# Optimization experiments

Hardware: AMD Instinct MI355X
Metric: run time of the kernel (lower is better)

## Reference

```python
import jax, jax.numpy as jnp
import numpy as np

THRESH = 1e-5   # replace_denormals threshold
EPS = 1e-5      # instance_norm eps

NUM_LAYERS, TOKEN_LEN, EMBED = 24, 100, 1024
N, B = 1025, 8  # seq (incl. cls token), batch


def _replace_denormals(x):
    return jnp.where((x < THRESH) & (x > -THRESH), THRESH, x)


def _delta_feat(feats, tokens, w_t2f, b_t2f, w_df, b_df, instance_norm):
    # feats: [n, b, c], tokens: [m, c]
    attn = jnp.einsum('nbc,mc->nbm', feats, tokens)
    if instance_norm:  # normalize over m per (n, b), biased variance (torch F.instance_norm)
        mu = attn.mean(axis=-1, keepdims=True)
        var = attn.var(axis=-1, keepdims=True)
        attn = (attn - mu) / jnp.sqrt(var + EPS)
    attn = jax.nn.softmax(attn * (feats.shape[-1] ** -0.5), axis=-1)
    v = tokens[1:] @ w_t2f.T + b_t2f                     # [m-1, c]
    df = jnp.einsum('nbm,mc->nbc', attn[:, :, 1:], v)    # drop first token column
    return (df + feats) @ w_df.T + b_df


def setup_inputs() -> dict:
    key = jax.random.key(0)
    ks = jax.random.split(key, 12)
    C = EMBED
    inp = {
        'feats': jax.random.normal(ks[0], (N, B, C), dtype=jnp.float32),
        'learnable_tokens': jax.random.normal(ks[1], (NUM_LAYERS, TOKEN_LEN, C), dtype=jnp.float32) * 0.04,
        'learnable_tokens2': jax.random.normal(ks[2], (NUM_LAYERS, TOKEN_LEN, C), dtype=jnp.float32) * 0.04,
        'w_t2f': jax.random.normal(ks[3], (C, C), dtype=jnp.float32) * 0.02,
        'b_t2f': jax.random.normal(ks[4], (C,), dtype=jnp.float32) * 0.02,
        'w_df': jax.random.normal(ks[5], (C, C), dtype=jnp.float32) * 0.02,
        'b_df': jax.random.normal(ks[6], (C,), dtype=jnp.float32) * 0.02,
        'w_t2f2': jax.random.normal(ks[7], (C, C), dtype=jnp.float32) * 0.02,
        'b_t2f2': jax.random.normal(ks[8], (C,), dtype=jnp.float32) * 0.02,
        'w_df2': jax.random.normal(ks[9], (C, C), dtype=jnp.float32) * 0.02,
        'b_df2': jax.random.normal(ks[10], (C,), dtype=jnp.float32) * 0.02,
        'scale': jnp.float32(0.001),
        'layer': 0,
    }
    return inp


def reference(feats, learnable_tokens, learnable_tokens2,
              w_t2f, b_t2f, w_df, b_df,
              w_t2f2, b_t2f2, w_df2, b_df2,
              scale, layer):
    # batch_first=False, has_cls_token=True (defaults)
    C = feats.shape[-1]
    cls_tok, x = feats[:1], feats[1:]            # [1,b,c], [n,b,c]
    n, b = x.shape[0], x.shape[1]

    # decompose: fft2 over last two dims (b, c), norm='backward'
    f = jnp.fft.fft2(x)
    re, im = jnp.real(f), jnp.imag(f)
    amp = jnp.sqrt(_replace_denormals(re * re + im * im))
    phase = jnp.arctan2(im, _replace_denormals(re))

    t1 = learnable_tokens[layer]
    t2 = learnable_tokens2[layer]
    d_phase = _delta_feat(phase, t1, w_t2f, b_t2f, w_df, b_df, instance_norm=False)
    d_amp = _delta_feat(amp, t2, w_t2f2, b_t2f2, w_df2, b_df2, instance_norm=True)

    # compose: stacked last dim has size 2, dim 2 has size C -> divide by sqrt(C*2)
    z = (jnp.cos(d_phase) * d_amp + 1j * (jnp.sin(d_phase) * d_amp)) / np.float32(np.sqrt(C * 2.0))
    z = z[..., : C // 2 + 1]                      # torch irfft2 trims last dim to s[-1]//2+1
    delta = jnp.fft.irfft2(z, s=(b, C), norm='ortho')

    out = x + delta * scale
    return jnp.concatenate([cls_tok, out], axis=0)
```

## Files before the change

### kernel.cpp

```cpp
#include <hip/hip_runtime.h>
#include <cstddef>


using bf16x8 = __attribute__((ext_vector_type(8))) short;
using f32x4  = __attribute__((ext_vector_type(4))) float;

__device__ inline short f2bf(float f) {
  union { float f; unsigned u; } v; v.f = f;
  unsigned r = v.u + 0x7FFFu + ((v.u >> 16) & 1u);
  return (short)(r >> 16);
}
__device__ inline float bf2f(short s) {
  union { unsigned u; float f; } v; v.u = ((unsigned)(unsigned short)s) << 16;
  return v.f;
}
__device__ inline void async16(const void* g, void* l) {
  __builtin_amdgcn_global_load_lds(
      (const __attribute__((address_space(1))) void*)g,
      (__attribute__((address_space(3))) void*)l, 16, 0, 0);
}
__device__ inline float fast_atan2(float y, float x) {
  float ax = fabsf(x), ay = fabsf(y);
  float mx = fmaxf(ax, ay), mn = fminf(ax, ay);
  float a = mn * __frcp_rn(mx);
  float s = a * a;
  float r = fmaf(fmaf(fmaf(-0.0464964749f, s, 0.15931422f), s, -0.327622764f),
                 s * a, a);
  if (ay > ax) r = 1.5707963267948966f - r;
  if (x < 0.f) r = 3.14159265358979f - r;
  return (y < 0.f) ? -r : r;
}

__device__ inline int PADi(int i) { return i + (i >> 5); }
__device__ inline int rev4_8(int t) {
  return ((t & 3) << 6) | (((t >> 2) & 3) << 4) | (((t >> 4) & 3) << 2) | ((t >> 6) & 3);
}

template <int SIGN>
__device__ inline void fft1024x4(float2 (*zb)[1056], int t) {
#pragma unroll
  for (int s = 0; s < 5; ++s) {
    const int Q = 256 >> (2 * s);
    const int j = t & (Q - 1);
    const int i0 = ((t & ~(Q - 1)) << 2) + j;
    const float ang = (float)SIGN * 6.283185307179586f * (float)j / (float)(4 * Q);
    float s1, c1; __sincosf(ang, &s1, &c1);
    const float c2 = c1 * c1 - s1 * s1, s2 = 2.f * c1 * s1;
    const float c3 = c2 * c1 - s2 * s1, s3 = c2 * s1 + s2 * c1;
#pragma unroll
    for (int p = 0; p < 4; ++p) {
      float2* z = zb[p];
      float2 x0 = z[PADi(i0)];
      float2 x1 = z[PADi(i0 + Q)];
      float2 x2 = z[PADi(i0 + 2 * Q)];
      float2 x3 = z[PADi(i0 + 3 * Q)];
      float t0x = x0.x + x2.x, t0y = x0.y + x2.y;
      float t1x = x0.x - x2.x, t1y = x0.y - x2.y;
      float t2x = x1.x + x3.x, t2y = x1.y + x3.y;
      float t3x = x1.x - x3.x, t3y = x1.y - x3.y;
      float u0x = t0x + t2x, u0y = t0y + t2y;
      float u2x = t0x - t2x, u2y = t0y - t2y;
      float u1x, u1y, u3x, u3y;
      if (SIGN < 0) { u1x = t1x + t3y; u1y = t1y - t3x; u3x = t1x - t3y; u3y = t1y + t3x; }
      else          { u1x = t1x - t3y; u1y = t1y + t3x; u3x = t1x + t3y; u3y = t1y - t3x; }
      z[PADi(i0)]         = make_float2(u0x, u0y);
      z[PADi(i0 + Q)]     = make_float2(u1x * c1 - u1y * s1, u1x * s1 + u1y * c1);
      z[PADi(i0 + 2 * Q)] = make_float2(u2x * c2 - u2y * s2, u2x * s2 + u2y * c2);
      z[PADi(i0 + 3 * Q)] = make_float2(u3x * c3 - u3y * s3, u3x * s3 + u3y * c3);
    }
    __syncthreads();
  }
}

__global__ __launch_bounds__(256) void fwd_fft2_amp(const float* __restrict__ feats,
                                                    short* __restrict__ ampb,
                                                    short* __restrict__ phaseb) {
  __shared__ float2 zb[4][1056];
  const int t = threadIdx.x;
  const int n = blockIdx.x;
  const float* base = feats + 8192 + (size_t)n * 8192;
#pragma unroll
  for (int p = 0; p < 4; ++p) {
    const float* x0 = base + (size_t)(2 * p) * 1024;
    const float* x1 = x0 + 1024;
#pragma unroll
    for (int m = 0; m < 4; ++m) {
      const int c = t + 256 * m;
      zb[p][PADi(c)] = make_float2(x0[c], x1[c]);
    }
  }
  __syncthreads();
  fft1024x4<-1>(zb, t);
  const int rt = rev4_8(t);
  const float cv[8] = {1.f, 0.70710678f, 0.f, -0.70710678f, -1.f, -0.70710678f, 0.f, 0.70710678f};
  const float sv[8] = {0.f, 0.70710678f, 1.f, 0.70710678f, 0.f, -0.70710678f, -1.f, -0.70710678f};
  short* ab = ampb + (size_t)n * 8192;
  short* pb = phaseb + (size_t)n * 8192;
#pragma unroll
  for (int m = 0; m < 4; ++m) {
    const int k = 256 * m + t;
    const int kk = (1024 - k) & 1023;
    const int pos  = 4 * rt + m;
    const int pos2 = 4 * rev4_8(kk & 255) + (kk >> 8);
    float xr[8], xi[8];
#pragma unroll
    for (int p = 0; p < 4; ++p) {
      float2 Z = zb[p][PADi(pos)];
      float2 W = zb[p][PADi(pos2)];
      xr[2 * p]     = 0.5f * (Z.x + W.x);
      xi[2 * p]     = 0.5f * (Z.y - W.y);
      xr[2 * p + 1] = 0.5f * (Z.y + W.y);
      xi[2 * p + 1] = 0.5f * (W.x - Z.x);
    }
#pragma unroll
    for (int kb = 0; kb < 8; ++kb) {
      float sr = 0.f, si = 0.f;
#pragma unroll
      for (int b = 0; b < 8; ++b) {
        const int p = (kb * b) & 7;
        sr += xr[b] * cv[p] + xi[b] * sv[p];
        si += xi[b] * cv[p] - xr[b] * sv[p];
      }
      float r2 = sr * sr + si * si;
      if (r2 < 1e-5f) r2 = 1e-5f;
      float a = sqrtf(r2);
      float rr = (sr < 1e-5f && sr > -1e-5f) ? 1e-5f : sr;
      float ph = fast_atan2(si, rr);
      ab[kb * 1024 + k] = f2bf(a);
      pb[kb * 1024 + k] = f2bf(ph);
    }
  }
}

__global__ __launch_bounds__(256) void conv_all(
    const float* __restrict__ w1, const float* __restrict__ w2,
    const float* __restrict__ w3, const float* __restrict__ w4,
    const float* __restrict__ lt1, const float* __restrict__ lt2,
    const int* __restrict__ layerp, const float* __restrict__ feats,
    short* __restrict__ Wdst, short* __restrict__ Tdst,
    float* __restrict__ out) {
  const int id = blockIdx.x;
  const int t = threadIdx.x * 4;
  if (id < 4096) {
    const int z = id >> 10, row = id & 1023;
    const float* W = (z == 0 ? w1 : z == 1 ? w2 : z == 2 ? w3 : w4)
                     + (size_t)row * 1024;
    short* D = Wdst + ((size_t)z * 1024 + row) * 1024;
    float4 v = *(const float4*)(W + t);
    D[t] = f2bf(v.x); D[t + 1] = f2bf(v.y); D[t + 2] = f2bf(v.z); D[t + 3] = f2bf(v.w);
  } else if (id < 4608) {
    const int i2 = id - 4096;
    const int zz = i2 >> 7, row = i2 & 127;
    const int z = zz & 1, shift = zz >> 1;
    short* D = Tdst + ((size_t)zz * 128 + row) * 1024;
    if (row + shift < 100) {
      const float* S = (z ? lt2 : lt1) + (size_t)layerp[0] * 102400
                       + (size_t)(row + shift) * 1024;
      float4 v = *(const float4*)(S + t);
      D[t] = f2bf(v.x); D[t + 1] = f2bf(v.y); D[t + 2] = f2bf(v.z); D[t + 3] = f2bf(v.w);
    } else {
      D[t] = 0; D[t + 1] = 0; D[t + 2] = 0; D[t + 3] = 0;
    }
  } else {
    const int i = (id - 4608) * 256 + threadIdx.x;
    out[i] = feats[i];
  }
}

__global__ __launch_bounds__(256) void gemm128(
    const short* A0, const short* A1,
    const short* B0, const short* B1,
    const short* Add0, const short* Add1,
    const float* bias0, const float* bias1,
    void* C0v, void* C1v,
    int K, int ldc, int outBf16, int biasMode) {
  const int z = blockIdx.z;
  const short* A   = z ? A1 : A0;
  const short* B   = z ? B1 : B0;
  const short* Add = z ? Add1 : Add0;
  const float* bias = z ? bias1 : bias0;
  void* Cv = z ? C1v : C0v;

  __shared__ __align__(16) short As[128 * 32];
  __shared__ __align__(16) short Bs[128 * 32];

  const int tid = threadIdx.x;
  const int wave = tid >> 6, lane = tid & 63;
  const int m16 = lane & 15, quad = lane >> 4;
  const int wm = (wave & 1) * 64, wn = (wave >> 1) * 64;

  f32x4 acc[4][4];
#pragma unroll
  for (int i = 0; i < 4; ++i)
#pragma unroll
    for (int j = 0; j < 4; ++j) acc[i][j] = (f32x4){0.f, 0.f, 0.f, 0.f};

  const int r0 = tid >> 2;
  const int csw = (((tid & 3) ^ ((r0 >> 1) & 3)) * 8);
  const short* aSrc0 = A + (size_t)(blockIdx.x * 128 + r0) * K + csw;
  const short* aSrc1 = aSrc0 + (size_t)64 * K;
  const short* bSrc0 = B + (size_t)(blockIdx.y * 128 + r0) * K + csw;
  const short* bSrc1 = bSrc0 + (size_t)64 * K;
  short* aDst0 = As + tid * 8;
  short* aDst1 = As + 2048 + tid * 8;
  short* bDst0 = Bs + tid * 8;
  short* bDst1 = Bs + 2048 + tid * 8;

  const int fcol = ((quad ^ ((m16 >> 1) & 3)) * 8) + m16 * 32;

  for (int k0 = 0; k0 < K; k0 += 32) {
    async16(aSrc0 + k0, aDst0);
    async16(aSrc1 + k0, aDst1);
    async16(bSrc0 + k0, bDst0);
    async16(bSrc1 + k0, bDst1);
    __syncthreads();
    bf16x8 af[4], bg[4];
#pragma unroll
    for (int ib = 0; ib < 4; ++ib)
      af[ib] = *(const bf16x8*)(As + (wm + ib * 16) * 32 + fcol);
#pragma unroll
    for (int jb = 0; jb < 4; ++jb)
      bg[jb] = *(const bf16x8*)(Bs + (wn + jb * 16) * 32 + fcol);
#pragma unroll
    for (int ib = 0; ib < 4; ++ib)
#pragma unroll
      for (int jb = 0; jb < 4; ++jb)
        acc[ib][jb] = __builtin_amdgcn_mfma_f32_16x16x32_bf16(af[ib], bg[jb], acc[ib][jb], 0, 0, 0);
    __syncthreads();
  }

#pragma unroll
  for (int ib = 0; ib < 4; ++ib) {
    const int rowb = blockIdx.x * 128 + wm + ib * 16 + quad * 4;
#pragma unroll
    for (int jb = 0; jb < 4; ++jb) {
      const int col = blockIdx.y * 128 + wn + jb * 16 + m16;
      const float bcv = (biasMode == 1) ? bias[col] : 0.f;
#pragma unroll
      for (int r = 0; r < 4; ++r) {
        const size_t idx = (size_t)(rowb + r) * (size_t)ldc + col;
        float v = acc[ib][jb][r] + bcv;
        if (biasMode == 2) v += bias[rowb + r];
        if (Add) v += bf2f(Add[idx]);
        if (outBf16) ((short*)Cv)[idx] = f2bf(v);
        else         ((float*)Cv)[idx] = v;
      }
    }
  }
}

__global__ __launch_bounds__(256) void gemm128_dual(
    const short* A1_0, const short* A1_1,
    const short* B1_0, const short* B1_1,
    const short* A2_0, const short* A2_1,
    const short* B2_0, const short* B2_1,
    const float* bias0, const float* bias1,
    short* C0, short* C1, int K1, int K2, int ldc) {
  const int z = blockIdx.z;
  const short* A1 = z ? A1_1 : A1_0;
  const short* B1 = z ? B1_1 : B1_0;
  const short* A2 = z ? A2_1 : A2_0;
  const short* B2 = z ? B2_1 : B2_0;
  const float* bias = z ? bias1 : bias0;
  short* C = z ? C1 : C0;

  __shared__ __align__(16) short As[128 * 32];
  __shared__ __align__(16) short Bs[128 * 32];

  const int tid = threadIdx.x;
  const int wave = tid >> 6, lane = tid & 63;
  const int m16 = lane & 15, quad = lane >> 4;
  const int wm = (wave & 1) * 64, wn = (wave >> 1) * 64;

  f32x4 acc[4][4];
#pragma unroll
  for (int i = 0; i < 4; ++i)
#pragma unroll
    for (int j = 0; j < 4; ++j) acc[i][j] = (f32x4){0.f, 0.f, 0.f, 0.f};

  const int r0 = tid >> 2;
  const int csw = (((tid & 3) ^ ((r0 >> 1) & 3)) * 8);
  short* aDst0 = As + tid * 8;
  short* aDst1 = As + 2048 + tid * 8;
  short* bDst0 = Bs + tid * 8;
  short* bDst1 = Bs + 2048 + tid * 8;
  const int fcol = ((quad ^ ((m16 >> 1) & 3)) * 8) + m16 * 32;

#pragma unroll 1
  for (int phase = 0; phase < 2; ++phase) {
    const short* A = phase ? A2 : A1;
    const short* B = phase ? B2 : B1;
    const int K = phase ? K2 : K1;
    const short* aSrc0 = A + (size_t)(blockIdx.x * 128 + r0) * K + csw;
    const short* aSrc1 = aSrc0 + (size_t)64 * K;
    const short* bSrc0 = B + (size_t)(blockIdx.y * 128 + r0) * K + csw;
    const short* bSrc1 = bSrc0 + (size_t)64 * K;
    for (int k0 = 0; k0 < K; k0 += 32) {
      async16(aSrc0 + k0, aDst0);
      async16(aSrc1 + k0, aDst1);
      async16(bSrc0 + k0, bDst0);
      async16(bSrc1 + k0, bDst1);
      __syncthreads();
      bf16x8 af[4], bg[4];
#pragma unroll
      for (int ib = 0; ib < 4; ++ib)
        af[ib] = *(const bf16x8*)(As + (wm + ib * 16) * 32 + fcol);
#pragma unroll
      for (int jb = 0; jb < 4; ++jb)
        bg[jb] = *(const bf16x8*)(Bs + (wn + jb * 16) * 32 + fcol);
#pragma unroll
      for (int ib = 0; ib < 4; ++ib)
#pragma unroll
        for (int jb = 0; jb < 4; ++jb)
          acc[ib][jb] = __builtin_amdgcn_mfma_f32_16x16x32_bf16(af[ib], bg[jb], acc[ib][jb], 0, 0, 0);
      __syncthreads();
    }
  }

#pragma unroll
  for (int ib = 0; ib < 4; ++ib) {
    const int rowb = blockIdx.x * 128 + wm + ib * 16 + quad * 4;
#pragma unroll
    for (int jb = 0; jb < 4; ++jb) {
      const int col = blockIdx.y * 128 + wn + jb * 16 + m16;
      const float bcv = bias[col];
#pragma unroll
      for (int r = 0; r < 4; ++r) {
        const size_t idx = (size_t)(rowb + r) * (size_t)ldc + col;
        C[idx] = f2bf(acc[ib][jb][r] + bcv);
      }
    }
  }
}

__global__ __launch_bounds__(256) void gemm64(
    const short* A0, const short* A1,
    const short* B0, const short* B1,
    const float* bias0, const float* bias1,
    void* C0v, void* C1v,
    int K, int ldc, int outBf16, int biasMode) {
  const int z = blockIdx.z;
  const short* A   = z ? A1 : A0;
  const short* B   = z ? B1 : B0;
  const float* bias = z ? bias1 : bias0;
  void* Cv = z ? C1v : C0v;

  __shared__ __align__(16) short As[64 * 32];
  __shared__ __align__(16) short Bs[128 * 32];

  const int tid = threadIdx.x;
  const int wave = tid >> 6, lane = tid & 63;
  const int m16 = lane & 15, quad = lane >> 4;
  const int wm = (wave & 1) * 32, wn = (wave >> 1) * 64;

  f32x4 acc[2][4];
#pragma unroll
  for (int i = 0; i < 2; ++i)
#pragma unroll
    for (int j = 0; j < 4; ++j) acc[i][j] = (f32x4){0.f, 0.f, 0.f, 0.f};

  const int r0 = tid >> 2;
  const int csw = (((tid & 3) ^ ((r0 >> 1) & 3)) * 8);
  const short* aSrc  = A + (size_t)(blockIdx.x * 64 + r0) * K + csw;
  const short* bSrc0 = B + (size_t)r0 * K + csw;
  const short* bSrc1 = bSrc0 + (size_t)64 * K;
  short* aDst  = As + tid * 8;
  short* bDst0 = Bs + tid * 8;
  short* bDst1 = Bs + 2048 + tid * 8;

  const int fcol = ((quad ^ ((m16 >> 1) & 3)) * 8) + m16 * 32;

  for (int k0 = 0; k0 < K; k0 += 32) {
    async16(aSrc + k0, aDst);
    async16(bSrc0 + k0, bDst0);
    async16(bSrc1 + k0, bDst1);
    __syncthreads();
    bf16x8 af[2], bg[4];
#pragma unroll
    for (int ib = 0; ib < 2; ++ib)
      af[ib] = *(const bf16x8*)(As + (wm + ib * 16) * 32 + fcol);
#pragma unroll
    for (int jb = 0; jb < 4; ++jb)
      bg[jb] = *(const bf16x8*)(Bs + (wn + jb * 16) * 32 + fcol);
#pragma unroll
    for (int ib = 0; ib < 2; ++ib)
#pragma unroll
      for (int jb = 0; jb < 4; ++jb)
        acc[ib][jb] = __builtin_amdgcn_mfma_f32_16x16x32_bf16(af[ib], bg[jb], acc[ib][jb], 0, 0, 0);
    __syncthreads();
  }

#pragma unroll
  for (int ib = 0; ib < 2; ++ib) {
    const int rowb = blockIdx.x * 64 + wm + ib * 16 + quad * 4;
#pragma unroll
    for (int jb = 0; jb < 4; ++jb) {
      const int col = wn + jb * 16 + m16;
      const float bcv = (biasMode == 1) ? bias[col] : 0.f;
#pragma unroll
      for (int r = 0; r < 4; ++r) {
        const size_t idx = (size_t)(rowb + r) * (size_t)ldc + col;
        float v = acc[ib][jb][r] + bcv;
        if (biasMode == 2) v += bias[rowb + r];
        if (outBf16) ((short*)Cv)[idx] = f2bf(v);
        else         ((float*)Cv)[idx] = v;
      }
    }
  }
}

__global__ __launch_bounds__(256) void gemm32_sm(
    const short* A0, const short* A1,
    const short* Tok,
    short* __restrict__ awb) {
  const int z = blockIdx.z;
  const short* A = z ? A1 : A0;
  const short* B = Tok + (size_t)z * 128 * 1024;
  const int K = 1024;

  __shared__ __align__(16) short As[32 * 32];
  __shared__ __align__(16) short Bs[128 * 32];
  __shared__ float ltile[32][129];
  __shared__ float red1[32][8], red2[32][8];

  const int tid = threadIdx.x;
  const int wave = tid >> 6, lane = tid & 63;
  const int m16 = lane & 15, quad = lane >> 4;
  const int wm = (wave & 1) * 16, wn = (wave >> 1) * 64;

  f32x4 acc[4];
#pragma unroll
  for (int j = 0; j < 4; ++j) acc[j] = (f32x4){0.f, 0.f, 0.f, 0.f};

  const int r0 = tid >> 2;
  const int csw = (((tid & 3) ^ ((r0 >> 1) & 3)) * 8);
  const short* aSrc  = A + (size_t)(blockIdx.x * 32 + r0) * K + csw;
  const short* bSrc0 = B + (size_t)r0 * K + csw;
  const short* bSrc1 = bSrc0 + (size_t)64 * K;
  short* aDst  = As + tid * 8;
  short* bDst0 = Bs + tid * 8;
  short* bDst1 = Bs + 2048 + tid * 8;
  const int fcol = ((quad ^ ((m16 >> 1) & 3)) * 8) + m16 * 32;

  for (int k0 = 0; k0 < K; k0 += 32) {
    if (tid < 128) async16(aSrc + k0, aDst);
    async16(bSrc0 + k0, bDst0);
    async16(bSrc1 + k0, bDst1);
    __syncthreads();
    bf16x8 af = *(const bf16x8*)(As + wm * 32 + fcol);
    bf16x8 bg[4];
#pragma unroll
    for (int jb = 0; jb < 4; ++jb)
      bg[jb] = *(const bf16x8*)(Bs + (wn + jb * 16) * 32 + fcol);
#pragma unroll
    for (int jb = 0; jb < 4; ++jb)
      acc[jb] = __builtin_amdgcn_mfma_f32_16x16x32_bf16(af, bg[jb], acc[jb], 0, 0, 0);
    __syncthreads();
  }

#pragma unroll
  for (int jb = 0; jb < 4; ++jb)
#pragma unroll
    for (int r = 0; r < 4; ++r)
      ltile[wm + quad * 4 + r][wn + jb * 16 + m16] = acc[jb][r];
  __syncthreads();

  const int row = tid >> 3, l8 = tid & 7;
  float s = 0.f, q = 0.f;
  for (int c = l8; c < 100; c += 8) { float x = ltile[row][c]; s += x; q += x * x; }
  red1[row][l8] = s; red2[row][l8] = q;
  __syncthreads();
  float ssum = 0.f, qsum = 0.f;
#pragma unroll
  for (int i = 0; i < 8; ++i) { ssum += red1[row][i]; qsum += red2[row][i]; }
  __syncthreads();
  const float mu = ssum * 0.01f;
  const float rinv = rsqrtf(fmaxf(qsum * 0.01f - mu * mu, 0.f) + 1e-5f);
  float mx = -3.4e38f;
  for (int c = l8; c < 100; c += 8) {
    float x = ltile[row][c];
    if (z == 1) x = (x - mu) * rinv;
    x *= 0.03125f;
    ltile[row][c] = x;
    mx = fmaxf(mx, x);
  }
  red1[row][l8] = mx;
  __syncthreads();
#pragma unroll
  for (int i = 0; i < 8; ++i) mx = fmaxf(mx, red1[row][i]);
  __syncthreads();
  float es = 0.f;
  for (int c = l8; c < 100; c += 8) {
    float e = __expf(ltile[row][c] - mx);
    ltile[row][c] = e; es += e;
  }
  red1[row][l8] = es;
  __syncthreads();
  float tot = 0.f;
#pragma unroll
  for (int i = 0; i < 8; ++i) tot += red1[row][i];
  const float inv = 1.f / tot;
  short* Aout = awb + ((size_t)z * 8192 + (size_t)blockIdx.x * 32 + row) * 128;
  for (int c = l8; c < 100; c += 8)
    if (c >= 1) Aout[c - 1] = f2bf(ltile[row][c] * inv);
  for (int k = l8; k < 128; k += 8)
    if (k >= 99) Aout[k] = 0;
}

__global__ __launch_bounds__(256) void inv_fft2_res(const short* __restrict__ dPb,
                                                    const short* __restrict__ dAb,
                                                    const float* __restrict__ feats,
                                                    const float* __restrict__ scalep,
                                                    float* __restrict__ out) {
  __shared__ float2 zb[4][1056];
  const int t = threadIdx.x;
  const int n = blockIdx.x;
  const short* pp = dPb + (size_t)n * 8192;
  const short* ap = dAb + (size_t)n * 8192;
  const float cv[8] = {1.f, 0.70710678f, 0.f, -0.70710678f, -1.f, -0.70710678f, 0.f, 0.70710678f};
  const float sv[8] = {0.f, 0.70710678f, 1.f, 0.70710678f, 0.f, -0.70710678f, -1.f, -0.70710678f};
  const float invs = 0.022097086912079608f;
  const float inv8 = 0.35355339059327373f;
  for (int k = t; k < 513; k += 256) {
    float zr[8], zi[8];
#pragma unroll
    for (int b = 0; b < 8; ++b) {
      float p = bf2f(pp[b * 1024 + k]);
      float a = bf2f(ap[b * 1024 + k]) * invs;
      float s, c; __sincosf(p, &s, &c);
      zr[b] = c * a; zi[b] = s * a;
    }
#pragma unroll
    for (int p4 = 0; p4 < 4; ++p4) {
      float2 a2, b2;
#pragma unroll
      for (int h = 0; h < 2; ++h) {
        const int bp = 2 * p4 + h;
        float sr = 0.f, si = 0.f;
#pragma unroll
        for (int b = 0; b < 8; ++b) {
          const int p = (bp * b) & 7;
          sr += zr[b] * cv[p] - zi[b] * sv[p];
          si += zi[b] * cv[p] + zr[b] * sv[p];
        }
        if (h == 0) a2 = make_float2(sr * inv8, si * inv8);
        else        b2 = make_float2(sr * inv8, si * inv8);
      }
      zb[p4][PADi(k)] = make_float2(a2.x - b2.y, a2.y + b2.x);
      if (k >= 1 && k <= 511)
        zb[p4][PADi(1024 - k)] = make_float2(a2.x + b2.y, b2.x - a2.y);
    }
  }
  __syncthreads();
  fft1024x4<1>(zb, t);
  const int rt = rev4_8(t);
  const float s = scalep[0] * 0.03125f;
#pragma unroll
  for (int p = 0; p < 4; ++p) {
    const size_t ob0 = 8192 + ((size_t)n * 8 + 2 * p) * 1024;
    const size_t ob1 = ob0 + 1024;
#pragma unroll
    for (int m = 0; m < 4; ++m) {
      const int nn = 256 * m + t;
      float2 y = zb[p][PADi(4 * rt + m)];
      out[ob0 + nn] = feats[ob0 + nn] + y.x * s;
      out[ob1 + nn] = feats[ob1 + nn] + y.y * s;
    }
  }
}

extern "C" void kernel_launch(void* const* d_in, const int* in_sizes, int n_in,
                              void* d_out, int out_size, void* d_ws, size_t ws_size,
                              hipStream_t stream) {
  const float* feats  = (const float*)d_in[0];
  const float* lt1    = (const float*)d_in[1];
  const float* lt2    = (const float*)d_in[2];
  const float* w_t2f  = (const float*)d_in[3];
  const float* b_t2f  = (const float*)d_in[4];
  const float* w_df   = (const float*)d_in[5];
  const float* b_df   = (const float*)d_in[6];
  const float* w_t2f2 = (const float*)d_in[7];
  const float* b_t2f2 = (const float*)d_in[8];
  const float* w_df2  = (const float*)d_in[9];
  const float* b_df2  = (const float*)d_in[10];
  const float* scalep = (const float*)d_in[11];
  const int*   layerp = (const int*)d_in[12];
  float* out = (float*)d_out;
  (void)in_sizes; (void)n_in; (void)out_size; (void)ws_size;

  const size_t SZ = 8192ull * 1024ull;
  short* Pa   = (short*)d_ws;
  short* Pb   = Pa + SZ;
  short* awb  = Pb + SZ;
  short* Tok  = awb + 2ull * 8192 * 128;
  short* Wall = Tok + 4ull * 128 * 1024;
  short* vrow = Wall + 4ull * 1024 * 1024;
  short* V2T  = vrow + 2ull * 128 * 1024;
  short* dP   = V2T + 2ull * 1024 * 128;
  short* dA   = dP + SZ;

  fwd_fft2_amp<<<dim3(1024), dim3(256), 0, stream>>>(feats, Pb, Pa);
  conv_all<<<dim3(4640), dim3(256), 0, stream>>>(
      w_t2f, w_t2f2, w_df, w_df2, lt1, lt2, layerp, feats, Wall, Tok, out);
  gemm32_sm<<<dim3(256, 1, 2), dim3(256), 0, stream>>>(Pa, Pb, Tok, awb);
  gemm128<<<dim3(1, 8, 2), dim3(256), 0, stream>>>(
      Tok + 2 * 128 * 1024, Tok + 3 * 128 * 1024, Wall, Wall + 1024 * 1024,
      (const short*)nullptr, (const short*)nullptr,
      b_t2f, b_t2f2, vrow, vrow + 128 * 1024, 1024, 1024, 1, 1);
  gemm64<<<dim3(16, 1, 2), dim3(256), 0, stream>>>(
      Wall + 2 * 1024 * 1024, Wall + 3 * 1024 * 1024,
      vrow, vrow + 128 * 1024,
      (const float*)nullptr, (const float*)nullptr,
      V2T, V2T + 1024 * 128, 1024, 128, 1, 0);
  gemm128_dual<<<dim3(64, 8, 2), dim3(256), 0, stream>>>(
      awb, awb + 8192 * 128, V2T, V2T + 1024 * 128,
      Pa, Pb, Wall + 2 * 1024 * 1024, Wall + 3 * 1024 * 1024,
      b_df, b_df2, dP, dA, 128, 1024, 1024);
  inv_fft2_res<<<dim3(1024), dim3(256), 0, stream>>>(dP, dA, feats, scalep, out);
}
```

Baseline: 291.4 us.

## Fuse conversion into FFT kernel, merge softmax and V GEMMs, use radix-8 butterflies

```diff
diff --git a/kernel.cpp b/kernel.cpp
--- a/kernel.cpp
+++ b/kernel.cpp
@@ -36,8 +36,55 @@
   return ((t & 3) << 6) | (((t >> 2) & 3) << 4) | (((t >> 4) & 3) << 2) | ((t >> 6) & 3);
 }
 
-template <int SIGN>
-__device__ inline void fft1024x4(float2 (*zb)[1056], int t) {
+__device__ inline void fft8_fwd(float* xr, float* xi) {
+  const float r = 0.70710678118654752f;
+  float ar[4], ai[4], br[4], bi[4], tr, ti;
+  ar[0]=xr[0]+xr[4]; ai[0]=xi[0]+xi[4]; br[0]=xr[0]-xr[4]; bi[0]=xi[0]-xi[4];
+  ar[1]=xr[1]+xr[5]; ai[1]=xi[1]+xi[5];
+  tr=xr[1]-xr[5]; ti=xi[1]-xi[5]; br[1]=(tr+ti)*r; bi[1]=(ti-tr)*r;
+  ar[2]=xr[2]+xr[6]; ai[2]=xi[2]+xi[6];
+  tr=xr[2]-xr[6]; ti=xi[2]-xi[6]; br[2]=ti; bi[2]=-tr;
+  ar[3]=xr[3]+xr[7]; ai[3]=xi[3]+xi[7];
+  tr=xr[3]-xr[7]; ti=xi[3]-xi[7]; br[3]=(ti-tr)*r; bi[3]=-(tr+ti)*r;
+  float u0r=ar[0]+ar[2], u0i=ai[0]+ai[2], u1r=ar[1]+ar[3], u1i=ai[1]+ai[3];
+  float v0r=ar[0]-ar[2], v0i=ai[0]-ai[2];
+  tr=ar[1]-ar[3]; ti=ai[1]-ai[3];
+  float v1r=ti, v1i=-tr;
+  xr[0]=u0r+u1r; xi[0]=u0i+u1i; xr[4]=u0r-u1r; xi[4]=u0i-u1i;
+  xr[2]=v0r+v1r; xi[2]=v0i+v1i; xr[6]=v0r-v1r; xi[6]=v0i-v1i;
+  u0r=br[0]+br[2]; u0i=bi[0]+bi[2]; u1r=br[1]+br[3]; u1i=bi[1]+bi[3];
+  v0r=br[0]-br[2]; v0i=bi[0]-bi[2];
+  tr=br[1]-br[3]; ti=bi[1]-bi[3];
+  v1r=ti; v1i=-tr;
+  xr[1]=u0r+u1r; xi[1]=u0i+u1i; xr[5]=u0r-u1r; xi[5]=u0i-u1i;
+  xr[3]=v0r+v1r; xi[3]=v0i+v1i; xr[7]=v0r-v1r; xi[7]=v0i-v1i;
+}
+__device__ inline void fft8_inv(float* xr, float* xi) {
+  const float r = 0.70710678118654752f;
+  float ar[4], ai[4], br[4], bi[4], tr, ti;
+  ar[0]=xr[0]+xr[4]; ai[0]=xi[0]+xi[4]; br[0]=xr[0]-xr[4]; bi[0]=xi[0]-xi[4];
+  ar[1]=xr[1]+xr[5]; ai[1]=xi[1]+xi[5];
+  tr=xr[1]-xr[5]; ti=xi[1]-xi[5]; br[1]=(tr-ti)*r; bi[1]=(tr+ti)*r;
+  ar[2]=xr[2]+xr[6]; ai[2]=xi[2]+xi[6];
+  tr=xr[2]-xr[6]; ti=xi[2]-xi[6]; br[2]=-ti; bi[2]=tr;
+  ar[3]=xr[3]+xr[7]; ai[3]=xi[3]+xi[7];
+  tr=xr[3]-xr[7]; ti=xi[3]-xi[7]; br[3]=-(tr+ti)*r; bi[3]=(tr-ti)*r;
+  float u0r=ar[0]+ar[2], u0i=ai[0]+ai[2], u1r=ar[1]+ar[3], u1i=ai[1]+ai[3];
+  float v0r=ar[0]-ar[2], v0i=ai[0]-ai[2];
+  tr=ar[1]-ar[3]; ti=ai[1]-ai[3];
+  float v1r=-ti, v1i=tr;
+  xr[0]=u0r+u1r; xi[0]=u0i+u1i; xr[4]=u0r-u1r; xi[4]=u0i-u1i;
+  xr[2]=v0r+v1r; xi[2]=v0i+v1i; xr[6]=v0r-v1r; xi[6]=v0i-v1i;
+  u0r=br[0]+br[2]; u0i=bi[0]+bi[2]; u1r=br[1]+br[3]; u1i=bi[1]+bi[3];
+  v0r=br[0]-br[2]; v0i=bi[0]-bi[2];
+  tr=br[1]-br[3]; ti=bi[1]-bi[3];
+  v1r=-ti; v1i=tr;
+  xr[1]=u0r+u1r; xi[1]=u0i+u1i; xr[5]=u0r-u1r; xi[5]=u0i-u1i;
+  xr[3]=v0r+v1r; xi[3]=v0i+v1i; xr[7]=v0r-v1r; xi[7]=v0i-v1i;
+}
+
+template <int SIGN, int NP>
+__device__ inline void fft1024xN(float2 (*zb)[1056], int t) {
 #pragma unroll
   for (int s = 0; s < 5; ++s) {
     const int Q = 256 >> (2 * s);
@@ -48,7 +95,7 @@
     const float c2 = c1 * c1 - s1 * s1, s2 = 2.f * c1 * s1;
     const float c3 = c2 * c1 - s2 * s1, s3 = c2 * s1 + s2 * c1;
 #pragma unroll
-    for (int p = 0; p < 4; ++p) {
+    for (int p = 0; p < NP; ++p) {
       float2* z = zb[p];
       float2 x0 = z[PADi(i0)];
       float2 x1 = z[PADi(i0 + Q)];
@@ -72,9 +119,44 @@
   }
 }
 
-__global__ __launch_bounds__(256) void fwd_fft2_amp(const float* __restrict__ feats,
-                                                    short* __restrict__ ampb,
-                                                    short* __restrict__ phaseb) {
+__global__ __launch_bounds__(256) void fwd_fft2_amp_conv(
+    const float* __restrict__ feats,
+    short* __restrict__ ampb, short* __restrict__ phaseb,
+    const float* __restrict__ w1, const float* __restrict__ w2,
+    const float* __restrict__ w3, const float* __restrict__ w4,
+    const float* __restrict__ lt1, const float* __restrict__ lt2,
+    const int* __restrict__ layerp,
+    short* __restrict__ Wdst, short* __restrict__ Tdst,
+    float* __restrict__ out) {
+  if (blockIdx.x >= 1024) {
+    const int id = blockIdx.x - 1024;
+    const int t4 = threadIdx.x * 4;
+    if (id < 4096) {
+      const int z = id >> 10, row = id & 1023;
+      const float* W = (z == 0 ? w1 : z == 1 ? w2 : z == 2 ? w3 : w4)
+                       + (size_t)row * 1024;
+      short* D = Wdst + ((size_t)z * 1024 + row) * 1024;
+      float4 v = *(const float4*)(W + t4);
+      D[t4] = f2bf(v.x); D[t4 + 1] = f2bf(v.y); D[t4 + 2] = f2bf(v.z); D[t4 + 3] = f2bf(v.w);
+    } else if (id < 4608) {
+      const int i2 = id - 4096;
+      const int zz = i2 >> 7, row = i2 & 127;
+      const int z = zz & 1, shift = zz >> 1;
+      short* D = Tdst + ((size_t)zz * 128 + row) * 1024;
+      if (row + shift < 100) {
+        const float* S = (z ? lt2 : lt1) + (size_t)layerp[0] * 102400
+                         + (size_t)(row + shift) * 1024;
+        float4 v = *(const float4*)(S + t4);
+        D[t4] = f2bf(v.x); D[t4 + 1] = f2bf(v.y); D[t4 + 2] = f2bf(v.z); D[t4 + 3] = f2bf(v.w);
+      } else {
+        D[t4] = 0; D[t4 + 1] = 0; D[t4 + 2] = 0; D[t4 + 3] = 0;
+      }
+    } else {
+      const int i = (id - 4608) * 256 + threadIdx.x;
+      out[i] = feats[i];
+    }
+    return;
+  }
   __shared__ float2 zb[4][1056];
   const int t = threadIdx.x;
   const int n = blockIdx.x;
@@ -90,10 +172,8 @@
     }
   }
   __syncthreads();
-  fft1024x4<-1>(zb, t);
+  fft1024xN<-1, 4>(zb, t);
   const int rt = rev4_8(t);
-  const float cv[8] = {1.f, 0.70710678f, 0.f, -0.70710678f, -1.f, -0.70710678f, 0.f, 0.70710678f};
-  const float sv[8] = {0.f, 0.70710678f, 1.f, 0.70710678f, 0.f, -0.70710678f, -1.f, -0.70710678f};
   short* ab = ampb + (size_t)n * 8192;
   short* pb = phaseb + (size_t)n * 8192;
 #pragma unroll
@@ -112,15 +192,10 @@
       xr[2 * p + 1] = 0.5f * (Z.y + W.y);
       xi[2 * p + 1] = 0.5f * (W.x - Z.x);
     }
+    fft8_fwd(xr, xi);
 #pragma unroll
     for (int kb = 0; kb < 8; ++kb) {
-      float sr = 0.f, si = 0.f;
-#pragma unroll
-      for (int b = 0; b < 8; ++b) {
-        const int p = (kb * b) & 7;
-        sr += xr[b] * cv[p] + xi[b] * sv[p];
-        si += xi[b] * cv[p] - xr[b] * sv[p];
-      }
+      float sr = xr[kb], si = xi[kb];
       float r2 = sr * sr + si * si;
       if (r2 < 1e-5f) r2 = 1e-5f;
       float a = sqrtf(r2);
@@ -132,119 +207,217 @@
   }
 }
 
-__global__ __launch_bounds__(256) void conv_all(
-    const float* __restrict__ w1, const float* __restrict__ w2,
-    const float* __restrict__ w3, const float* __restrict__ w4,
-    const float* __restrict__ lt1, const float* __restrict__ lt2,
-    const int* __restrict__ layerp, const float* __restrict__ feats,
-    short* __restrict__ Wdst, short* __restrict__ Tdst,
-    float* __restrict__ out) {
-  const int id = blockIdx.x;
-  const int t = threadIdx.x * 4;
-  if (id < 4096) {
-    const int z = id >> 10, row = id & 1023;
-    const float* W = (z == 0 ? w1 : z == 1 ? w2 : z == 2 ? w3 : w4)
-                     + (size_t)row * 1024;
-    short* D = Wdst + ((size_t)z * 1024 + row) * 1024;
-    float4 v = *(const float4*)(W + t);
-    D[t] = f2bf(v.x); D[t + 1] = f2bf(v.y); D[t + 2] = f2bf(v.z); D[t + 3] = f2bf(v.w);
-  } else if (id < 4608) {
-    const int i2 = id - 4096;
-    const int zz = i2 >> 7, row = i2 & 127;
-    const int z = zz & 1, shift = zz >> 1;
-    short* D = Tdst + ((size_t)zz * 128 + row) * 1024;
-    if (row + shift < 100) {
-      const float* S = (z ? lt2 : lt1) + (size_t)layerp[0] * 102400
-                       + (size_t)(row + shift) * 1024;
-      float4 v = *(const float4*)(S + t);
-      D[t] = f2bf(v.x); D[t + 1] = f2bf(v.y); D[t + 2] = f2bf(v.z); D[t + 3] = f2bf(v.w);
-    } else {
-      D[t] = 0; D[t + 1] = 0; D[t + 2] = 0; D[t + 3] = 0;
-    }
-  } else {
-    const int i = (id - 4608) * 256 + threadIdx.x;
-    out[i] = feats[i];
-  }
-}
-
-__global__ __launch_bounds__(256) void gemm128(
+__global__ __launch_bounds__(256) void gemm_sm_v(
     const short* A0, const short* A1,
-    const short* B0, const short* B1,
-    const short* Add0, const short* Add1,
-    const float* bias0, const float* bias1,
-    void* C0v, void* C1v,
-    int K, int ldc, int outBf16, int biasMode) {
+    const short* Tok,
+    const short* Wall,
+    const float* bt1, const float* bt2,
+    short* __restrict__ awb,
+    short* __restrict__ vrow) {
+  __shared__ __align__(16) char smem[28800];
   const int z = blockIdx.z;
-  const short* A   = z ? A1 : A0;
-  const short* B   = z ? B1 : B0;
-  const short* Add = z ? Add1 : Add0;
-  const float* bias = z ? bias1 : bias0;
-  void* Cv = z ? C1v : C0v;
-
-  __shared__ __align__(16) short As[128 * 32];
-  __shared__ __align__(16) short Bs[128 * 32];
-
   const int tid = threadIdx.x;
   const int wave = tid >> 6, lane = tid & 63;
   const int m16 = lane & 15, quad = lane >> 4;
-  const int wm = (wave & 1) * 64, wn = (wave >> 1) * 64;
-
-  f32x4 acc[4][4];
-#pragma unroll
-  for (int i = 0; i < 4; ++i)
-#pragma unroll
-    for (int j = 0; j < 4; ++j) acc[i][j] = (f32x4){0.f, 0.f, 0.f, 0.f};
-
+  const int fcol = ((quad ^ ((m16 >> 1) & 3)) * 8) + m16 * 32;
   const int r0 = tid >> 2;
   const int csw = (((tid & 3) ^ ((r0 >> 1) & 3)) * 8);
-  const short* aSrc0 = A + (size_t)(blockIdx.x * 128 + r0) * K + csw;
-  const short* aSrc1 = aSrc0 + (size_t)64 * K;
-  const short* bSrc0 = B + (size_t)(blockIdx.y * 128 + r0) * K + csw;
+
+  if (blockIdx.x >= 256) {
+    const int jb = blockIdx.x - 256;
+    const short* A = Tok + (size_t)(2 + z) * 128 * 1024;
+    const short* B = Wall + (size_t)z * 1024 * 1024;
+    const float* bias = z ? bt2 : bt1;
+    short* C = vrow + (size_t)z * 128 * 1024;
+    const int K = 1024;
+    short* As = (short*)smem;
+    short* Bs = (short*)(smem + 8192);
+    const int wm = (wave & 1) * 64, wn = (wave >> 1) * 64;
+    f32x4 acc[4][4];
+#pragma unroll
+    for (int i = 0; i < 4; ++i)
+#pragma unroll
+      for (int j = 0; j < 4; ++j) acc[i][j] = (f32x4){0.f, 0.f, 0.f, 0.f};
+    const short* aSrc0 = A + (size_t)r0 * K + csw;
+    const short* aSrc1 = aSrc0 + (size_t)64 * K;
+    const short* bSrc0 = B + (size_t)(jb * 128 + r0) * K + csw;
+    const short* bSrc1 = bSrc0 + (size_t)64 * K;
+    short* aDst0 = As + tid * 8;
+    short* aDst1 = As + 2048 + tid * 8;
+    short* bDst0 = Bs + tid * 8;
+    short* bDst1 = Bs + 2048 + tid * 8;
+    for (int k0 = 0; k0 < K; k0 += 32) {
+      async16(aSrc0 + k0, aDst0);
+      async16(aSrc1 + k0, aDst1);
+      async16(bSrc0 + k0, bDst0);
+      async16(bSrc1 + k0, bDst1);
+      __syncthreads();
+      bf16x8 af[4], bg[4];
+#pragma unroll
+      for (int ib = 0; ib < 4; ++ib)
+        af[ib] = *(const bf16x8*)(As + (wm + ib * 16) * 32 + fcol);
+#pragma unroll
+      for (int jb2 = 0; jb2 < 4; ++jb2)
+        bg[jb2] = *(const bf16x8*)(Bs + (wn + jb2 * 16) * 32 + fcol);
+#pragma unroll
+      for (int ib = 0; ib < 4; ++ib)
+#pragma unroll
+        for (int jb2 = 0; jb2 < 4; ++jb2)
+          acc[ib][jb2] = __builtin_amdgcn_mfma_f32_16x16x32_bf16(af[ib], bg[jb2], acc[ib][jb2], 0, 0, 0);
+      __syncthreads();
+    }
+#pragma unroll
+    for (int ib = 0; ib < 4; ++ib) {
+      const int rowb = wm + ib * 16 + quad * 4;
+#pragma unroll
+      for (int jb2 = 0; jb2 < 4; ++jb2) {
+        const int col = jb * 128 + wn + jb2 * 16 + m16;
+        const float bcv = bias[col];
+#pragma unroll
+        for (int r = 0; r < 4; ++r)
+          C[(size_t)(rowb + r) * 1024 + col] = f2bf(acc[ib][jb2][r] + bcv);
+      }
+    }
+    return;
+  }
+
+  const short* A = z ? A1 : A0;
+  const short* B = Tok + (size_t)z * 128 * 1024;
+  const int K = 1024;
+  short* As = (short*)smem;
+  short* Bs = (short*)(smem + 2048);
+  float (*ltile)[129] = (float(*)[129])(smem + 10240);
+  float (*red1)[8] = (float(*)[8])(smem + 26752);
+  float (*red2)[8] = (float(*)[8])(smem + 27776);
+  const int wm = (wave & 1) * 16, wn = (wave >> 1) * 64;
+  f32x4 acc[4];
+#pragma unroll
+  for (int j = 0; j < 4; ++j) acc[j] = (f32x4){0.f, 0.f, 0.f, 0.f};
+  const short* aSrc  = A + (size_t)(blockIdx.x * 32 + r0) * K + csw;
+  const short* bSrc0 = B + (size_t)r0 * K + csw;
   const short* bSrc1 = bSrc0 + (size_t)64 * K;
-  short* aDst0 = As + tid * 8;
-  short* aDst1 = As + 2048 + tid * 8;
+  short* aDst  = As + tid * 8;
   short* bDst0 = Bs + tid * 8;
   short* bDst1 = Bs + 2048 + tid * 8;
-
-  const int fcol = ((quad ^ ((m16 >> 1) & 3)) * 8) + m16 * 32;
-
   for (int k0 = 0; k0 < K; k0 += 32) {
-    async16(aSrc0 + k0, aDst0);
-    async16(aSrc1 + k0, aDst1);
+    if (tid < 128) async16(aSrc + k0, aDst);
     async16(bSrc0 + k0, bDst0);
     async16(bSrc1 + k0, bDst1);
     __syncthreads();
-    bf16x8 af[4], bg[4];
-#pragma unroll
-    for (int ib = 0; ib < 4; ++ib)
-      af[ib] = *(const bf16x8*)(As + (wm + ib * 16) * 32 + fcol);
+    bf16x8 af = *(const bf16x8*)(As + wm * 32 + fcol);
+    bf16x8 bg[4];
 #pragma unroll
     for (int jb = 0; jb < 4; ++jb)
       bg[jb] = *(const bf16x8*)(Bs + (wn + jb * 16) * 32 + fcol);
 #pragma unroll
-    for (int ib = 0; ib < 4; ++ib)
+    for (int jb = 0; jb < 4; ++jb)
+      acc[jb] = __builtin_amdgcn_mfma_f32_16x16x32_bf16(af, bg[jb], acc[jb], 0, 0, 0);
+    __syncthreads();
+  }
+#pragma unroll
+  for (int jb = 0; jb < 4; ++jb)
+#pragma unroll
+    for (int r = 0; r < 4; ++r)
+      ltile[wm + quad * 4 + r][wn + jb * 16 + m16] = acc[jb][r];
+  __syncthreads();
+  const int row = tid >> 3, l8 = tid & 7;
+  float s = 0.f, q = 0.f;
+  for (int c = l8; c < 100; c += 8) { float x = ltile[row][c]; s += x; q += x * x; }
+  red1[row][l8] = s; red2[row][l8] = q;
+  __syncthreads();
+  float ssum = 0.f, qsum = 0.f;
+#pragma unroll
+  for (int i = 0; i < 8; ++i) { ssum += red1[row][i]; qsum += red2[row][i]; }
+  __syncthreads();
+  const float mu = ssum * 0.01f;
+  const float rinv = rsqrtf(fmaxf(qsum * 0.01f - mu * mu, 0.f) + 1e-5f);
+  float mx = -3.4e38f;
+  for (int c = l8; c < 100; c += 8) {
+    float x = ltile[row][c];
+    if (z == 1) x = (x - mu) * rinv;
+    x *= 0.03125f;
+    ltile[row][c] = x;
+    mx = fmaxf(mx, x);
+  }
+  red1[row][l8] = mx;
+  __syncthreads();
+#pragma unroll
+  for (int i = 0; i < 8; ++i) mx = fmaxf(mx, red1[row][i]);
+  __syncthreads();
+  float es = 0.f;
+  for (int c = l8; c < 100; c += 8) {
+    float e = __expf(ltile[row][c] - mx);
+    ltile[row][c] = e; es += e;
+  }
+  red1[row][l8] = es;
+  __syncthreads();
+  float tot = 0.f;
+#pragma unroll
+  for (int i = 0; i < 8; ++i) tot += red1[row][i];
+  const float inv = 1.f / tot;
+  short* Aout = awb + ((size_t)z * 8192 + (size_t)blockIdx.x * 32 + row) * 128;
+  for (int c = l8; c < 100; c += 8)
+    if (c >= 1) Aout[c - 1] = f2bf(ltile[row][c] * inv);
+  for (int k = l8; k < 128; k += 8)
+    if (k >= 99) Aout[k] = 0;
+}
+
+__global__ __launch_bounds__(256) void gemm64(
+    const short* A0, const short* A1,
+    const short* B0, const short* B1,
+    void* C0v, void* C1v, int K, int ldc) {
+  const int z = blockIdx.z;
+  const short* A = z ? A1 : A0;
+  const short* B = z ? B1 : B0;
+  void* Cv = z ? C1v : C0v;
+  __shared__ __align__(16) short As[64 * 32];
+  __shared__ __align__(16) short Bs[128 * 32];
+  const int tid = threadIdx.x;
+  const int wave = tid >> 6, lane = tid & 63;
+  const int m16 = lane & 15, quad = lane >> 4;
+  const int wm = (wave & 1) * 32, wn = (wave >> 1) * 64;
+  f32x4 acc[2][4];
+#pragma unroll
+  for (int i = 0; i < 2; ++i)
+#pragma unroll
+    for (int j = 0; j < 4; ++j) acc[i][j] = (f32x4){0.f, 0.f, 0.f, 0.f};
+  const int r0 = tid >> 2;
+  const int csw = (((tid & 3) ^ ((r0 >> 1) & 3)) * 8);
+  const short* aSrc  = A + (size_t)(blockIdx.x * 64 + r0) * K + csw;
+  const short* bSrc0 = B + (size_t)r0 * K + csw;
+  const short* bSrc1 = bSrc0 + (size_t)64 * K;
+  short* aDst  = As + tid * 8;
+  short* bDst0 = Bs + tid * 8;
+  short* bDst1 = Bs + 2048 + tid * 8;
+  const int fcol = ((quad ^ ((m16 >> 1) & 3)) * 8) + m16 * 32;
+  for (int k0 = 0; k0 < K; k0 += 32) {
+    async16(aSrc + k0, aDst);
+    async16(bSrc0 + k0, bDst0);
+    async16(bSrc1 + k0, bDst1);
+    __syncthreads();
+    bf16x8 af[2], bg[4];
+#pragma unroll
+    for (int ib = 0; ib < 2; ++ib)
+      af[ib] = *(const bf16x8*)(As + (wm + ib * 16) * 32 + fcol);
+#pragma unroll
+    for (int jb = 0; jb < 4; ++jb)
+      bg[jb] = *(const bf16x8*)(Bs + (wn + jb * 16) * 32 + fcol);
+#pragma unroll
+    for (int ib = 0; ib < 2; ++ib)
 #pragma unroll
       for (int jb = 0; jb < 4; ++jb)
         acc[ib][jb] = __builtin_amdgcn_mfma_f32_16x16x32_bf16(af[ib], bg[jb], acc[ib][jb], 0, 0, 0);
     __syncthreads();
   }
-
-#pragma unroll
-  for (int ib = 0; ib < 4; ++ib) {
-    const int rowb = blockIdx.x * 128 + wm + ib * 16 + quad * 4;
+#pragma unroll
+  for (int ib = 0; ib < 2; ++ib) {
+    const int rowb = blockIdx.x * 64 + wm + ib * 16 + quad * 4;
 #pragma unroll
     for (int jb = 0; jb < 4; ++jb) {
-      const int col = blockIdx.y * 128 + wn + jb * 16 + m16;
-      const float bcv = (biasMode == 1) ? bias[col] : 0.f;
-#pragma unroll
-      for (int r = 0; r < 4; ++r) {
-        const size_t idx = (size_t)(rowb + r) * (size_t)ldc + col;
-        float v = acc[ib][jb][r] + bcv;
-        if (biasMode == 2) v += bias[rowb + r];
-        if (Add) v += bf2f(Add[idx]);
-        if (outBf16) ((short*)Cv)[idx] = f2bf(v);
-        else         ((float*)Cv)[idx] = v;
-      }
+      const int col = wn + jb * 16 + m16;
+#pragma unroll
+      for (int r = 0; r < 4; ++r)
+        ((short*)Cv)[(size_t)(rowb + r) * ldc + col] = f2bf(acc[ib][jb][r]);
     }
   }
 }
@@ -263,21 +436,17 @@
   const short* B2 = z ? B2_1 : B2_0;
   const float* bias = z ? bias1 : bias0;
   short* C = z ? C1 : C0;
-
   __shared__ __align__(16) short As[128 * 32];
   __shared__ __align__(16) short Bs[128 * 32];
-
   const int tid = threadIdx.x;
   const int wave = tid >> 6, lane = tid & 63;
   const int m16 = lane & 15, quad = lane >> 4;
   const int wm = (wave & 1) * 64, wn = (wave >> 1) * 64;
-
   f32x4 acc[4][4];
 #pragma unroll
   for (int i = 0; i < 4; ++i)
 #pragma unroll
     for (int j = 0; j < 4; ++j) acc[i][j] = (f32x4){0.f, 0.f, 0.f, 0.f};
-
   const int r0 = tid >> 2;
   const int csw = (((tid & 3) ^ ((r0 >> 1) & 3)) * 8);
   short* aDst0 = As + tid * 8;
@@ -285,7 +454,6 @@
   short* bDst0 = Bs + tid * 8;
   short* bDst1 = Bs + 2048 + tid * 8;
   const int fcol = ((quad ^ ((m16 >> 1) & 3)) * 8) + m16 * 32;
-
 #pragma unroll 1
   for (int phase = 0; phase < 2; ++phase) {
     const short* A = phase ? A2 : A1;
@@ -316,7 +484,6 @@
       __syncthreads();
     }
   }
-
 #pragma unroll
   for (int ib = 0; ib < 4; ++ib) {
     const int rowb = blockIdx.x * 128 + wm + ib * 16 + quad * 4;
@@ -331,180 +498,6 @@
       }
     }
   }
-}
-
-__global__ __launch_bounds__(256) void gemm64(
-    const short* A0, const short* A1,
-    const short* B0, const short* B1,
-    const float* bias0, const float* bias1,
-    void* C0v, void* C1v,
-    int K, int ldc, int outBf16, int biasMode) {
-  const int z = blockIdx.z;
-  const short* A   = z ? A1 : A0;
-  const short* B   = z ? B1 : B0;
-  const float* bias = z ? bias1 : bias0;
-  void* Cv = z ? C1v : C0v;
-
-  __shared__ __align__(16) short As[64 * 32];
-  __shared__ __align__(16) short Bs[128 * 32];
-
-  const int tid = threadIdx.x;
-  const int wave = tid >> 6, lane = tid & 63;
-  const int m16 = lane & 15, quad = lane >> 4;
-  const int wm = (wave & 1) * 32, wn = (wave >> 1) * 64;
-
-  f32x4 acc[2][4];
-#pragma unroll
-  for (int i = 0; i < 2; ++i)
-#pragma unroll
-    for (int j = 0; j < 4; ++j) acc[i][j] = (f32x4){0.f, 0.f, 0.f, 0.f};
-
-  const int r0 = tid >> 2;
-  const int csw = (((tid & 3) ^ ((r0 >> 1) & 3)) * 8);
-  const short* aSrc  = A + (size_t)(blockIdx.x * 64 + r0) * K + csw;
-  const short* bSrc0 = B + (size_t)r0 * K + csw;
-  const short* bSrc1 = bSrc0 + (size_t)64 * K;
-  short* aDst  = As + tid * 8;
-  short* bDst0 = Bs + tid * 8;
-  short* bDst1 = Bs + 2048 + tid * 8;
-
-  const int fcol = ((quad ^ ((m16 >> 1) & 3)) * 8) + m16 * 32;
-
-  for (int k0 = 0; k0 < K; k0 += 32) {
-    async16(aSrc + k0, aDst);
-    async16(bSrc0 + k0, bDst0);
-    async16(bSrc1 + k0, bDst1);
-    __syncthreads();
-    bf16x8 af[2], bg[4];
-#pragma unroll
-    for (int ib = 0; ib < 2; ++ib)
-      af[ib] = *(const bf16x8*)(As + (wm + ib * 16) * 32 + fcol);
-#pragma unroll
-    for (int jb = 0; jb < 4; ++jb)
-      bg[jb] = *(const bf16x8*)(Bs + (wn + jb * 16) * 32 + fcol);
-#pragma unroll
-    for (int ib = 0; ib < 2; ++ib)
-#pragma unroll
-      for (int jb = 0; jb < 4; ++jb)
-        acc[ib][jb] = __builtin_amdgcn_mfma_f32_16x16x32_bf16(af[ib], bg[jb], acc[ib][jb], 0, 0, 0);
-    __syncthreads();
-  }
-
-#pragma unroll
-  for (int ib = 0; ib < 2; ++ib) {
-    const int rowb = blockIdx.x * 64 + wm + ib * 16 + quad * 4;
-#pragma unroll
-    for (int jb = 0; jb < 4; ++jb) {
-      const int col = wn + jb * 16 + m16;
-      const float bcv = (biasMode == 1) ? bias[col] : 0.f;
-#pragma unroll
-      for (int r = 0; r < 4; ++r) {
-        const size_t idx = (size_t)(rowb + r) * (size_t)ldc + col;
-        float v = acc[ib][jb][r] + bcv;
-        if (biasMode == 2) v += bias[rowb + r];
-        if (outBf16) ((short*)Cv)[idx] = f2bf(v);
-        else         ((float*)Cv)[idx] = v;
-      }
-    }
-  }
-}
-
-__global__ __launch_bounds__(256) void gemm32_sm(
-    const short* A0, const short* A1,
-    const short* Tok,
-    short* __restrict__ awb) {
-  const int z = blockIdx.z;
-  const short* A = z ? A1 : A0;
-  const short* B = Tok + (size_t)z * 128 * 1024;
-  const int K = 1024;
-
-  __shared__ __align__(16) short As[32 * 32];
-  __shared__ __align__(16) short Bs[128 * 32];
-  __shared__ float ltile[32][129];
-  __shared__ float red1[32][8], red2[32][8];
-
-  const int tid = threadIdx.x;
-  const int wave = tid >> 6, lane = tid & 63;
-  const int m16 = lane & 15, quad = lane >> 4;
-  const int wm = (wave & 1) * 16, wn = (wave >> 1) * 64;
-
-  f32x4 acc[4];
-#pragma unroll
-  for (int j = 0; j < 4; ++j) acc[j] = (f32x4){0.f, 0.f, 0.f, 0.f};
-
-  const int r0 = tid >> 2;
-  const int csw = (((tid & 3) ^ ((r0 >> 1) & 3)) * 8);
-  const short* aSrc  = A + (size_t)(blockIdx.x * 32 + r0) * K + csw;
-  const short* bSrc0 = B + (size_t)r0 * K + csw;
-  const short* bSrc1 = bSrc0 + (size_t)64 * K;
-  short* aDst  = As + tid * 8;
-  short* bDst0 = Bs + tid * 8;
-  short* bDst1 = Bs + 2048 + tid * 8;
-  const int fcol = ((quad ^ ((m16 >> 1) & 3)) * 8) + m16 * 32;
-
-  for (int k0 = 0; k0 < K; k0 += 32) {
-    if (tid < 128) async16(aSrc + k0, aDst);
-    async16(bSrc0 + k0, bDst0);
-    async16(bSrc1 + k0, bDst1);
-    __syncthreads();
-    bf16x8 af = *(const bf16x8*)(As + wm * 32 + fcol);
-    bf16x8 bg[4];
-#pragma unroll
-    for (int jb = 0; jb < 4; ++jb)
-      bg[jb] = *(const bf16x8*)(Bs + (wn + jb * 16) * 32 + fcol);
-#pragma unroll
-    for (int jb = 0; jb < 4; ++jb)
-      acc[jb] = __builtin_amdgcn_mfma_f32_16x16x32_bf16(af, bg[jb], acc[jb], 0, 0, 0);
-    __syncthreads();
-  }
-
-#pragma unroll
-  for (int jb = 0; jb < 4; ++jb)
-#pragma unroll
-    for (int r = 0; r < 4; ++r)
-      ltile[wm + quad * 4 + r][wn + jb * 16 + m16] = acc[jb][r];
-  __syncthreads();
-
-  const int row = tid >> 3, l8 = tid & 7;
-  float s = 0.f, q = 0.f;
-  for (int c = l8; c < 100; c += 8) { float x = ltile[row][c]; s += x; q += x * x; }
-  red1[row][l8] = s; red2[row][l8] = q;
-  __syncthreads();
-  float ssum = 0.f, qsum = 0.f;
-#pragma unroll
-  for (int i = 0; i < 8; ++i) { ssum += red1[row][i]; qsum += red2[row][i]; }
-  __syncthreads();
-  const float mu = ssum * 0.01f;
-  const float rinv = rsqrtf(fmaxf(qsum * 0.01f - mu * mu, 0.f) + 1e-5f);
-  float mx = -3.4e38f;
-  for (int c = l8; c < 100; c += 8) {
-    float x = ltile[row][c];
-    if (z == 1) x = (x - mu) * rinv;
-    x *= 0.03125f;
-    ltile[row][c] = x;
-    mx = fmaxf(mx, x);
-  }
-  red1[row][l8] = mx;
-  __syncthreads();
-#pragma unroll
-  for (int i = 0; i < 8; ++i) mx = fmaxf(mx, red1[row][i]);
-  __syncthreads();
-  float es = 0.f;
-  for (int c = l8; c < 100; c += 8) {
-    float e = __expf(ltile[row][c] - mx);
-    ltile[row][c] = e; es += e;
-  }
-  red1[row][l8] = es;
-  __syncthreads();
-  float tot = 0.f;
-#pragma unroll
-  for (int i = 0; i < 8; ++i) tot += red1[row][i];
-  const float inv = 1.f / tot;
-  short* Aout = awb + ((size_t)z * 8192 + (size_t)blockIdx.x * 32 + row) * 128;
-  for (int c = l8; c < 100; c += 8)
-    if (c >= 1) Aout[c - 1] = f2bf(ltile[row][c] * inv);
-  for (int k = l8; k < 128; k += 8)
-    if (k >= 99) Aout[k] = 0;
 }
 
 __global__ __launch_bounds__(256) void inv_fft2_res(const short* __restrict__ dPb,
@@ -512,13 +505,11 @@
                                                     const float* __restrict__ feats,
                                                     const float* __restrict__ scalep,
                                                     float* __restrict__ out) {
-  __shared__ float2 zb[4][1056];
+  __shared__ float2 zb[2][1056];
   const int t = threadIdx.x;
-  const int n = blockIdx.x;
+  const int n = blockIdx.x >> 1, q = blockIdx.x & 1;
   const short* pp = dPb + (size_t)n * 8192;
   const short* ap = dAb + (size_t)n * 8192;
-  const float cv[8] = {1.f, 0.70710678f, 0.f, -0.70710678f, -1.f, -0.70710678f, 0.f, 0.70710678f};
-  const float sv[8] = {0.f, 0.70710678f, 1.f, 0.70710678f, 0.f, -0.70710678f, -1.f, -0.70710678f};
   const float invs = 0.022097086912079608f;
   const float inv8 = 0.35355339059327373f;
   for (int k = t; k < 513; k += 256) {
@@ -530,39 +521,30 @@
       float s, c; __sincosf(p, &s, &c);
       zr[b] = c * a; zi[b] = s * a;
     }
-#pragma unroll
-    for (int p4 = 0; p4 < 4; ++p4) {
-      float2 a2, b2;
-#pragma unroll
-      for (int h = 0; h < 2; ++h) {
-        const int bp = 2 * p4 + h;
-        float sr = 0.f, si = 0.f;
-#pragma unroll
-        for (int b = 0; b < 8; ++b) {
-          const int p = (bp * b) & 7;
-          sr += zr[b] * cv[p] - zi[b] * sv[p];
-          si += zi[b] * cv[p] + zr[b] * sv[p];
-        }
-        if (h == 0) a2 = make_float2(sr * inv8, si * inv8);
-        else        b2 = make_float2(sr * inv8, si * inv8);
-      }
-      zb[p4][PADi(k)] = make_float2(a2.x - b2.y, a2.y + b2.x);
+    fft8_inv(zr, zi);
+#pragma unroll
+    for (int l = 0; l < 2; ++l) {
+      const int bp = 4 * q + 2 * l;
+      float ax = zr[bp] * inv8,     ay = zi[bp] * inv8;
+      float bx = zr[bp + 1] * inv8, by = zi[bp + 1] * inv8;
+      zb[l][PADi(k)] = make_float2(ax - by, ay + bx);
       if (k >= 1 && k <= 511)
-        zb[p4][PADi(1024 - k)] = make_float2(a2.x + b2.y, b2.x - a2.y);
-    }
-  }
-  __syncthreads();
-  fft1024x4<1>(zb, t);
+        zb[l][PADi(1024 - k)] = make_float2(ax + by, bx - ay);
+    }
+  }
+  __syncthreads();
+  fft1024xN<1, 2>(zb, t);
   const int rt = rev4_8(t);
   const float s = scalep[0] * 0.03125f;
 #pragma unroll
-  for (int p = 0; p < 4; ++p) {
-    const size_t ob0 = 8192 + ((size_t)n * 8 + 2 * p) * 1024;
+  for (int l = 0; l < 2; ++l) {
+    const int p4 = 2 * q + l;
+    const size_t ob0 = 8192 + ((size_t)n * 8 + 2 * p4) * 1024;
     const size_t ob1 = ob0 + 1024;
 #pragma unroll
     for (int m = 0; m < 4; ++m) {
       const int nn = 256 * m + t;
-      float2 y = zb[p][PADi(4 * rt + m)];
+      float2 y = zb[l][PADi(4 * rt + m)];
       out[ob0 + nn] = feats[ob0 + nn] + y.x * s;
       out[ob1 + nn] = feats[ob1 + nn] + y.y * s;
     }
@@ -599,22 +581,18 @@
   short* dP   = V2T + 2ull * 1024 * 128;
   short* dA   = dP + SZ;
 
-  fwd_fft2_amp<<<dim3(1024), dim3(256), 0, stream>>>(feats, Pb, Pa);
-  conv_all<<<dim3(4640), dim3(256), 0, stream>>>(
-      w_t2f, w_t2f2, w_df, w_df2, lt1, lt2, layerp, feats, Wall, Tok, out);
-  gemm32_sm<<<dim3(256, 1, 2), dim3(256), 0, stream>>>(Pa, Pb, Tok, awb);
-  gemm128<<<dim3(1, 8, 2), dim3(256), 0, stream>>>(
-      Tok + 2 * 128 * 1024, Tok + 3 * 128 * 1024, Wall, Wall + 1024 * 1024,
-      (const short*)nullptr, (const short*)nullptr,
-      b_t2f, b_t2f2, vrow, vrow + 128 * 1024, 1024, 1024, 1, 1);
+  fwd_fft2_amp_conv<<<dim3(5664), dim3(256), 0, stream>>>(
+      feats, Pb, Pa, w_t2f, w_t2f2, w_df, w_df2, lt1, lt2, layerp,
+      Wall, Tok, out);
+  gemm_sm_v<<<dim3(264, 1, 2), dim3(256), 0, stream>>>(
+      Pa, Pb, Tok, Wall, b_t2f, b_t2f2, awb, vrow);
   gemm64<<<dim3(16, 1, 2), dim3(256), 0, stream>>>(
       Wall + 2 * 1024 * 1024, Wall + 3 * 1024 * 1024,
       vrow, vrow + 128 * 1024,
-      (const float*)nullptr, (const float*)nullptr,
-      V2T, V2T + 1024 * 128, 1024, 128, 1, 0);
+      V2T, V2T + 1024 * 128, 1024, 128);
   gemm128_dual<<<dim3(64, 8, 2), dim3(256), 0, stream>>>(
       awb, awb + 8192 * 128, V2T, V2T + 1024 * 128,
       Pa, Pb, Wall + 2 * 1024 * 1024, Wall + 3 * 1024 * 1024,
       b_df, b_df2, dP, dA, 128, 1024, 1024);
-  inv_fft2_res<<<dim3(1024), dim3(256), 0, stream>>>(dP, dA, feats, scalep, out);
-}
+  inv_fft2_res<<<dim3(2048), dim3(256), 0, stream>>>(dP, dA, feats, scalep, out);
+}
```

After: 270.4 us. -7.2%, faster.
